# Optimization experiments

Measured on AMD Instinct MI355X. Metric: run time of the kernel, lower is better.

## Reference

```python
import math
import jax, jax.numpy as jnp
import numpy as np

G, NP, L = 256, 24, 3            # graphs, atoms per graph, GPS layers
C, TDIM, NFREQ, NT = 256, 256, 10, 100
EDIM = NFREQ * 2 * 3 + 9         # SinusoidsEmbedding.dim + lattice_input_dim = 69
N = G * NP                       # 6144 nodes
H = 4                            # attention heads


def _silu(x):
    return x * jax.nn.sigmoid(x)


def _bn(x, g, b):
    # BatchNorm1d, training-mode batch statistics (biased var), eps=1e-5
    m = x.mean(0)
    v = ((x - m) ** 2).mean(0)
    return (x - m) * jax.lax.rsqrt(v + 1e-5) * g + b


def _forward(t, frac_coords, lattice, type_emb, node_align_W, node_align_b,
             gine_edge_W, gine_edge_b, gine_W1, gine_b1, gine_W2, gine_b2,
             attn_in_W, attn_in_b, attn_out_W, attn_out_b,
             mlp_W1, mlp_b1, mlp_W2, mlp_b2,
             bn1_g, bn1_b, bn2_g, bn2_b, bn3_g, bn3_b, ln_g, ln_b,
             tro_W1, tro_b1, tro_W2, tro_b2,
             lat_W1, lat_b1, lat_W2, lat_b2, lat_W3,
             fc_W1, fc_b1, fc_W2, fc_b2, fc_W3,
             atom_types, node2graph, edge_src, edge_dst):
    # sinusoidal time embedding [G, TDIM], repeated per node
    half = TDIM // 2
    tf = jnp.exp(jnp.arange(half, dtype=jnp.float32) * (-math.log(10000.0) / (half - 1)))
    te = t[:, None] * tf[None, :]
    te = jnp.concatenate([jnp.sin(te), jnp.cos(te)], -1)
    time_emb = jnp.repeat(te, NP, axis=0)                      # [N, TDIM]
    x = jnp.concatenate([type_emb[atom_types], time_emb], 1) @ node_align_W + node_align_b

    # edge features: sinusoids of periodic frac diff + per-graph lattice
    fd = (frac_coords[edge_dst] - frac_coords[edge_src]) % 1.0  # [E,3]
    sf = 2.0 * math.pi * jnp.arange(NFREQ, dtype=jnp.float32)
    emb = (fd[..., None] * sf).reshape(-1, 3 * NFREQ)
    eattr = jnp.concatenate([jnp.sin(emb), jnp.cos(emb), lattice[node2graph[edge_src]]], 1)

    scale = 1.0 / math.sqrt(C // H)
    for l in range(L):
        # --- GINEConv: gather -> relu(x_j + edge_emb) -> scatter-add -> MLP ---
        eemb = eattr @ gine_edge_W[l] + gine_edge_b[l]          # [E, C]
        msg = jax.nn.relu(x[edge_src] + eemb)
        aggr = jax.ops.segment_sum(msg, edge_dst, num_segments=N)
        z = x + aggr                                            # (1+eps)*x, eps=0
        z = _silu(z @ gine_W1[l] + gine_b1[l]) @ gine_W2[l] + gine_b2[l]
        h1 = _bn(z + x, bn1_g[l], bn1_b[l])
        # --- dense-batched multihead self-attention (all graphs have NP nodes) ---
        xd = x.reshape(G, NP, C)
        qkv = xd @ attn_in_W[l] + attn_in_b[l]
        q, k, v = jnp.split(qkv, 3, axis=-1)
        q = q.reshape(G, NP, H, C // H).transpose(0, 2, 1, 3)
        k = k.reshape(G, NP, H, C // H).transpose(0, 2, 1, 3)
        v = v.reshape(G, NP, H, C // H).transpose(0, 2, 1, 3)
        a = jax.nn.softmax(jnp.einsum('ghqd,ghkd->ghqk', q, k) * scale, axis=-1)
        o = jnp.einsum('ghqk,ghkd->ghqd', a, v).transpose(0, 2, 1, 3).reshape(G, NP, C)
        o = (o @ attn_out_W[l] + attn_out_b[l]).reshape(N, C)
        h2 = _bn(o + x, bn2_g[l], bn2_b[l])
        # --- combine + MLP (GPSConv default: ReLU, dropout=0) ---
        out = h1 + h2
        out = out + jax.nn.relu(out @ mlp_W1[l] + mlp_b1[l]) @ mlp_W2[l] + mlp_b2[l]
        x = _bn(out, bn3_g[l], bn3_b[l])

    # final LayerNorm over feature dim
    m = x.mean(-1, keepdims=True)
    v = ((x - m) ** 2).mean(-1, keepdims=True)
    hn = (x - m) * jax.lax.rsqrt(v + 1e-5) * ln_g + ln_b

    # scatter-mean graph pooling
    cnt = jax.ops.segment_sum(jnp.ones((N, 1), hn.dtype), node2graph, num_segments=G)
    gf = jax.ops.segment_sum(hn, node2graph, num_segments=G) / cnt

    types_pred = _silu(hn @ tro_W1 + tro_b1) @ tro_W2 + tro_b2
    lattice_pred = _silu(_silu(gf @ lat_W1 + lat_b1) @ lat_W2 + lat_b2) @ lat_W3
    frac_pred = _silu(_silu(hn @ fc_W1 + fc_b1) @ fc_W2 + fc_b2) @ fc_W3
    return types_pred, lattice_pred, frac_pred


def setup_inputs() -> dict:
    key = jax.random.key(0)
    ki = iter(jax.random.split(key, 40))

    def nrm(shape, s=0.02):
        return jax.random.normal(next(ki), shape, jnp.float32) * s

    # block-diagonal fully-connected edges, dense_to_sparse row-major order
    g = np.repeat(np.arange(G), NP * NP)
    i = np.tile(np.repeat(np.arange(NP), NP), G)
    j = np.tile(np.tile(np.arange(NP), NP), G)
    inp = {
        "t": jax.random.uniform(next(ki), (G,), jnp.float32),
        "frac_coords": jax.random.uniform(next(ki), (N, 3), jnp.float32),
        "lattice": nrm((G, 9), 1.0),
        "type_emb": nrm((NT, C)),
        "node_align_W": nrm((C + TDIM, C)), "node_align_b": jnp.zeros((C,), jnp.float32),
        "gine_edge_W": nrm((L, EDIM, C)), "gine_edge_b": jnp.zeros((L, C), jnp.float32),
        "gine_W1": nrm((L, C, C)), "gine_b1": jnp.zeros((L, C), jnp.float32),
        "gine_W2": nrm((L, C, C)), "gine_b2": jnp.zeros((L, C), jnp.float32),
        "attn_in_W": nrm((L, C, 3 * C)), "attn_in_b": jnp.zeros((L, 3 * C), jnp.float32),
        "attn_out_W": nrm((L, C, C)), "attn_out_b": jnp.zeros((L, C), jnp.float32),
        "mlp_W1": nrm((L, C, 2 * C)), "mlp_b1": jnp.zeros((L, 2 * C), jnp.float32),
        "mlp_W2": nrm((L, 2 * C, C)), "mlp_b2": jnp.zeros((L, C), jnp.float32),
        "bn1_g": jnp.ones((L, C), jnp.float32), "bn1_b": jnp.zeros((L, C), jnp.float32),
        "bn2_g": jnp.ones((L, C), jnp.float32), "bn2_b": jnp.zeros((L, C), jnp.float32),
        "bn3_g": jnp.ones((L, C), jnp.float32), "bn3_b": jnp.zeros((L, C), jnp.float32),
        "ln_g": jnp.ones((C,), jnp.float32), "ln_b": jnp.zeros((C,), jnp.float32),
        "tro_W1": nrm((C, C // 2)), "tro_b1": jnp.zeros((C // 2,), jnp.float32),
        "tro_W2": nrm((C // 2, NT)), "tro_b2": jnp.zeros((NT,), jnp.float32),
        "lat_W1": nrm((C, C // 2)), "lat_b1": jnp.zeros((C // 2,), jnp.float32),
        "lat_W2": nrm((C // 2, C // 4)), "lat_b2": jnp.zeros((C // 4,), jnp.float32),
        "lat_W3": nrm((C // 4, 9)),
        "fc_W1": nrm((C, C // 2)), "fc_b1": jnp.zeros((C // 2,), jnp.float32),
        "fc_W2": nrm((C // 2, C // 4)), "fc_b2": jnp.zeros((C // 4,), jnp.float32),
        "fc_W3": nrm((C // 4, 3)),
        "atom_types": jax.random.randint(next(ki), (N,), 0, NT, jnp.int32),
        "node2graph": jnp.asarray(np.repeat(np.arange(G), NP), jnp.int32),
        "edge_src": jnp.asarray(g * NP + i, jnp.int32),
        "edge_dst": jnp.asarray(g * NP + j, jnp.int32),
    }
    return inp


def reference(t, frac_coords, lattice, type_emb, node_align_W, node_align_b,
              gine_edge_W, gine_edge_b, gine_W1, gine_b1, gine_W2, gine_b2,
              attn_in_W, attn_in_b, attn_out_W, attn_out_b,
              mlp_W1, mlp_b1, mlp_W2, mlp_b2,
              bn1_g, bn1_b, bn2_g, bn2_b, bn3_g, bn3_b, ln_g, ln_b,
              tro_W1, tro_b1, tro_W2, tro_b2,
              lat_W1, lat_b1, lat_W2, lat_b2, lat_W3,
              fc_W1, fc_b1, fc_W2, fc_b2, fc_W3,
              atom_types, node2graph, edge_src, edge_dst):
    return _forward(t, frac_coords, lattice, type_emb, node_align_W, node_align_b,
                    gine_edge_W, gine_edge_b, gine_W1, gine_b1, gine_W2, gine_b2,
                    attn_in_W, attn_in_b, attn_out_W, attn_out_b,
                    mlp_W1, mlp_b1, mlp_W2, mlp_b2,
                    bn1_g, bn1_b, bn2_g, bn2_b, bn3_g, bn3_b, ln_g, ln_b,
                    tro_W1, tro_b1, tro_W2, tro_b2,
                    lat_W1, lat_b1, lat_W2, lat_b2, lat_W3,
                    fc_W1, fc_b1, fc_W2, fc_b2, fc_W3,
                    atom_types, node2graph, edge_src, edge_dst)
```

## Files before the change

### kernel.cpp

```cpp
#include <hip/hip_runtime.h>
#include <hip/hip_bf16.h>
#include <math.h>

#define GG 256
#define NP 24
#define LL 3
#define CC 256
#define NN (GG*NP)
#define HH 4
#define DH 64

typedef __hip_bfloat16 bf;
typedef __attribute__((ext_vector_type(8))) short bfrag;
typedef __attribute__((ext_vector_type(4))) float ffrag;

__device__ __forceinline__ short pk(float x) {
    union { bf h; short s; } u; u.h = __float2bfloat16(x); return u.s;
}
__device__ __forceinline__ float b2f_s(short x) {
    union { short s; bf h; } u; u.s = x; return __bfloat162float(u.h);
}

typedef __attribute__((address_space(1))) const void gv_t;
typedef __attribute__((address_space(3))) void lv_t;

__global__ void signal_k(float* out, int n, float val) {
    int i = blockIdx.x * 256 + threadIdx.x;
    if (i < n) out[i] = val;
}

#define ETAB_ELEMS (GG * 24 * 24 * 64)
#define GEWTAB_BLKS (192 + (ETAB_ELEMS + 255) / 256)
#define BUILDA_BLKS ((NN * 512 + 255) / 256)

struct TArgs {
    const float* src[9];
    long dstOff[9];
    int K[9], N[9], L[9];
    int blk0[10];
};

__global__ void prep_all(TArgs a, bf* __restrict__ wt,
                         const float* __restrict__ geW, short* __restrict__ wh,
                         short* __restrict__ wl, const float* __restrict__ frac,
                         short* __restrict__ eh, short* __restrict__ el,
                         const float* __restrict__ t,
                         const float* __restrict__ type_emb,
                         const unsigned int* __restrict__ atoms,
                         float* __restrict__ A) {
    __shared__ int ok;
    int bid = blockIdx.x;
    int nT = a.blk0[9];
    if (bid < nT) {
        int s = 0;
        while (s < 8 && bid >= a.blk0[s + 1]) ++s;
        long idx = (long)(bid - a.blk0[s]) * 256 + threadIdx.x;
        int KN = a.K[s] * a.N[s];
        long sz = (long)KN * a.L[s];
        if (idx >= sz) return;
        int l = (int)(idx / KN);
        int rem = (int)(idx % KN);
        int k = rem / a.N[s], n = rem % a.N[s];
        wt[a.dstOff[s] + (long)l * KN + (long)n * a.K[s] + k] =
            __float2bfloat16(a.src[s][idx]);
    } else if (bid < nT + GEWTAB_BLKS) {
        int b2 = bid - nT;
        if (b2 < 192) {
            int idx = b2 * 256 + threadIdx.x;
            if (idx >= 49152) return;
            int k = idx & 63;
            int n = (idx >> 6) & 127;
            int half = (idx >> 13) & 1;
            int l = idx >> 14;
            float v = (k < 60) ? geW[(long)l * 69 * 256 + (long)k * 256 + half * 128 + n] : 0.f;
            short hi = pk(v);
            short lo = pk(v - b2f_s(hi));
            wh[idx] = hi;
            wl[idx] = lo;
        } else {
            int idx = (b2 - 192) * 256 + threadIdx.x;
            if (idx >= ETAB_ELEMS) return;
            int k = idx & 63;
            int rem = idx >> 6;
            int i = rem % 24;
            int rem2 = rem / 24;
            int j = rem2 % 24;
            int g = rem2 / 24;
            float val = 0.f;
            if (k < 60) {
                int r = (k < 30) ? k : k - 30;
                int d = r / 10, f = r % 10;
                float fd = frac[g * 72 + j * 3 + d] - frac[g * 72 + i * 3 + d];
                fd -= floorf(fd);
                float ang = 6.283185307179586f * (float)f * fd;
                val = (k < 30) ? sinf(ang) : cosf(ang);
            }
            short hi = pk(val);
            eh[idx] = hi;
            el[idx] = pk(val - b2f_s(hi));
        }
    } else {
        int b3 = bid - nT - GEWTAB_BLKS;
        if (threadIdx.x == 0) ok = 1;
        __syncthreads();
        if (atoms[2 * threadIdx.x + 1] != 0u) ok = 0;
        __syncthreads();
        int i64 = ok;
        int idx = b3 * 256 + threadIdx.x;
        if (idx >= NN * 512) return;
        int n = idx >> 9;
        int k = idx & 511;
        if (k < 256) {
            int aidx = i64 ? (int)atoms[2 * n] : (int)atoms[n];
            A[idx] = type_emb[(long)aidx * CC + k];
        } else {
            int d = k - 256;
            int g = n / NP;
            float tv = t[g];
            int dd = (d < 128) ? d : d - 128;
            float tf = expf(dd * (-9.210340371976184f / 127.0f));
            float ang = tv * tf;
            A[idx] = (d < 128) ? sinf(ang) : cosf(ang);
        }
    }
}

__global__ __launch_bounds__(256) void gemm_mfma(
        const float* __restrict__ A, const bf* __restrict__ Wt,
        const float* __restrict__ bias, const float* __restrict__ bias2,
        const float* __restrict__ res,
        float* __restrict__ C, int M, int K, int N, int act) {
    __shared__ __align__(16) short As[2][32 * 72];
    __shared__ __align__(16) short Bs[2][2][64 * 32];
    int tid = threadIdx.x;
    int lane = tid & 63, w = tid >> 6;
    int wm = w & 1, wn = w >> 1;
    int m0 = blockIdx.x * 32, n0 = blockIdx.y * 64;
    ffrag acc[2] = {};
    int sa_m = tid >> 3, sa_k = (tid & 7) << 3;
    int fr_row = lane & 15, quad = lane >> 4, fr_k = quad << 3;
    int brow = w * 16 + (lane >> 2);
    int bko = (lane & 3) << 3;
    const short* wsrc = (const short*)Wt + (long)(n0 + brow) * K + bko;

    {
        const float* Ap = A + (long)(m0 + sa_m) * K + sa_k;
        float4 a1 = *(const float4*)Ap;
        float4 a2 = *(const float4*)(Ap + 4);
        __builtin_amdgcn_global_load_lds((gv_t*)(wsrc), (lv_t*)(&Bs[0][0][w * 512]), 16, 0, 0);
        __builtin_amdgcn_global_load_lds((gv_t*)(wsrc + 32), (lv_t*)(&Bs[0][1][w * 512]), 16, 0, 0);
        short* ap = &As[0][sa_m * 72 + sa_k];
        ap[0] = pk(a1.x); ap[1] = pk(a1.y); ap[2] = pk(a1.z); ap[3] = pk(a1.w);
        ap[4] = pk(a2.x); ap[5] = pk(a2.y); ap[6] = pk(a2.z); ap[7] = pk(a2.w);
    }
    __syncthreads();

    int nk = K >> 6;
    int cur = 0;
    for (int i = 0; i < nk; ++i) {
        float4 a1n, a2n;
        bool more = (i + 1) < nk;
        if (more) {
            int kn = (i + 1) << 6;
            __builtin_amdgcn_global_load_lds((gv_t*)(wsrc + kn),
                (lv_t*)(&Bs[cur ^ 1][0][w * 512]), 16, 0, 0);
            __builtin_amdgcn_global_load_lds((gv_t*)(wsrc + kn + 32),
                (lv_t*)(&Bs[cur ^ 1][1][w * 512]), 16, 0, 0);
            const float* Ap = A + (long)(m0 + sa_m) * K + kn + sa_k;
            a1n = *(const float4*)Ap;
            a2n = *(const float4*)(Ap + 4);
        }
        bfrag af0  = *(const bfrag*)(&As[cur][(wm * 16 + fr_row) * 72 + fr_k]);
        bfrag af1  = *(const bfrag*)(&As[cur][(wm * 16 + fr_row) * 72 + 32 + fr_k]);
        bfrag bg00 = *(const bfrag*)(&Bs[cur][0][(wn * 32 + fr_row) * 32 + fr_k]);
        bfrag bg01 = *(const bfrag*)(&Bs[cur][0][(wn * 32 + 16 + fr_row) * 32 + fr_k]);
        bfrag bg10 = *(const bfrag*)(&Bs[cur][1][(wn * 32 + fr_row) * 32 + fr_k]);
        bfrag bg11 = *(const bfrag*)(&Bs[cur][1][(wn * 32 + 16 + fr_row) * 32 + fr_k]);
        acc[0] = __builtin_amdgcn_mfma_f32_16x16x32_bf16(af0, bg00, acc[0], 0, 0, 0);
        acc[1] = __builtin_amdgcn_mfma_f32_16x16x32_bf16(af0, bg01, acc[1], 0, 0, 0);
        acc[0] = __builtin_amdgcn_mfma_f32_16x16x32_bf16(af1, bg10, acc[0], 0, 0, 0);
        acc[1] = __builtin_amdgcn_mfma_f32_16x16x32_bf16(af1, bg11, acc[1], 0, 0, 0);
        if (more) {
            short* ap = &As[cur ^ 1][sa_m * 72 + sa_k];
            ap[0] = pk(a1n.x); ap[1] = pk(a1n.y); ap[2] = pk(a1n.z); ap[3] = pk(a1n.w);
            ap[4] = pk(a2n.x); ap[5] = pk(a2n.y); ap[6] = pk(a2n.z); ap[7] = pk(a2n.w);
        }
        __syncthreads();
        cur ^= 1;
    }

    int mbase = (lane >> 4) << 2;
#pragma unroll
    for (int nt = 0; nt < 2; ++nt) {
        int n = n0 + wn * 32 + nt * 16 + (lane & 15);
        float bv = bias ? ((bias2 && n >= 128) ? bias2[n - 128] : bias[n]) : 0.f;
#pragma unroll
        for (int r = 0; r < 4; ++r) {
            int m = m0 + wm * 16 + mbase + r;
            float v = acc[nt][r] + bv;
            if (act == 1) v = fmaxf(v, 0.f);
            else if (act == 2) v = v / (1.f + expf(-v));
            if (res) v += res[(long)m * N + n];
            C[(long)m * N + n] = v;
        }
    }
}

__device__ __forceinline__ void gemm_k_body(
        const float* __restrict__ A, int lda, int mA0,
        const float* __restrict__ W, const float* __restrict__ bias,
        float* __restrict__ Cf, int ldc, int mOut0,
        int n0, int K, int Nc, int act,
        float (*Asf)[64], float (*Bsf)[64], int tid) {
    int tx = tid & 15, ty = tid >> 4;
    float acc[4][4] = {{0.f}};
    int am = tid >> 2;
    int ak = (tid & 3) << 3;
    int bk = tid >> 4;
    int bn = (tid & 15) << 2;

    for (int k0 = 0; k0 < K; k0 += 32) {
        const float* Ap = A + (long)(mA0 + am) * lda + k0 + ak;
        float4 a1 = *(const float4*)Ap;
        float4 a2 = *(const float4*)(Ap + 4);
        float w1[4], w2[4];
#pragma unroll
        for (int u = 0; u < 4; ++u) {
            int n = n0 + bn + u;
            w1[u] = (n < Nc) ? W[(long)(k0 + bk) * Nc + n] : 0.f;
            w2[u] = (n < Nc) ? W[(long)(k0 + bk + 16) * Nc + n] : 0.f;
        }
        __syncthreads();
        Asf[ak + 0][am] = a1.x; Asf[ak + 1][am] = a1.y;
        Asf[ak + 2][am] = a1.z; Asf[ak + 3][am] = a1.w;
        Asf[ak + 4][am] = a2.x; Asf[ak + 5][am] = a2.y;
        Asf[ak + 6][am] = a2.z; Asf[ak + 7][am] = a2.w;
#pragma unroll
        for (int u = 0; u < 4; ++u) {
            Bsf[bk][bn + u] = w1[u];
            Bsf[bk + 16][bn + u] = w2[u];
        }
        __syncthreads();
#pragma unroll
        for (int k = 0; k < 32; ++k) {
            float4 a = *(const float4*)(&Asf[k][ty << 2]);
            float4 b = *(const float4*)(&Bsf[k][tx << 2]);
            acc[0][0] += a.x * b.x; acc[0][1] += a.x * b.y; acc[0][2] += a.x * b.z; acc[0][3] += a.x * b.w;
            acc[1][0] += a.y * b.x; acc[1][1] += a.y * b.y; acc[1][2] += a.y * b.z; acc[1][3] += a.y * b.w;
            acc[2][0] += a.z * b.x; acc[2][1] += a.z * b.y; acc[2][2] += a.z * b.z; acc[2][3] += a.z * b.w;
            acc[3][0] += a.w * b.x; acc[3][1] += a.w * b.y; acc[3][2] += a.w * b.z; acc[3][3] += a.w * b.w;
        }
    }
#pragma unroll
    for (int i = 0; i < 4; ++i) {
        int m = mOut0 + (ty << 2) + i;
#pragma unroll
        for (int j = 0; j < 4; ++j) {
            int n = n0 + (tx << 2) + j;
            if (n >= Nc) continue;
            float v = acc[i][j];
            if (bias) v += bias[n];
            if (act == 1) v = fmaxf(v, 0.f);
            else if (act == 2) v = v / (1.f + expf(-v));
            Cf[(long)m * ldc + n] = v;
        }
    }
}

__global__ __launch_bounds__(256) void tail_k(
        const float* __restrict__ s2, const float* __restrict__ s1,
        const float* __restrict__ W30, const float* __restrict__ b31,
        const float* __restrict__ W39, const float* __restrict__ b40,
        const float* __restrict__ W41,
        const float* __restrict__ lw1, const float* __restrict__ lb1,
        const float* __restrict__ lw2, const float* __restrict__ lb2,
        const float* __restrict__ lw3,
        float* __restrict__ out_types, float* __restrict__ out_lat,
        float* __restrict__ out_frac) {
    __shared__ __align__(16) float Asf[32][64];
    __shared__ __align__(16) float Bsf[32][64];
    __shared__ __align__(16) float Imm[64][64];
    __shared__ float gfl[256];
    __shared__ float h1s[128];
    __shared__ float h2s[64];
    int tid = threadIdx.x;
    int b = blockIdx.x;
    if (b < 192) {
        int bx = b >> 1, by = b & 1;
        gemm_k_body(s2, 256, bx * 64, W30, b31, out_types, 100, bx * 64,
                    by * 64, 128, 100, 0, Asf, Bsf, tid);
    } else if (b < 288) {
        int m0 = (b - 192) * 64;
        gemm_k_body(s2 + 128, 256, m0, W39, b40, &Imm[0][0], 64, 0,
                    0, 128, 64, 2, Asf, Bsf, tid);
        __syncthreads();
        gemm_k_body(&Imm[0][0], 64, 0, W41, nullptr, out_frac, 3, m0,
                    0, 64, 3, 0, Asf, Bsf, tid);
    } else {
        int g = b - 288, t = tid;
        {
            float s = 0.f;
            for (int j = 0; j < NP; ++j) s += s1[(long)(g * NP + j) * CC + t];
            gfl[t] = s * (1.f / 24.f);
        }
        __syncthreads();
        if (t < 128) {
            float acc = 0.f;
            for (int k = 0; k < 256; ++k) acc += gfl[k] * lw1[k * 128 + t];
            float v = acc;
            v += lb1[t];
            v = v / (1.f + expf(-v));
            h1s[t] = v;
        }
        __syncthreads();
        if (t < 64) {
            float acc = 0.f;
            for (int k = 0; k < 128; ++k) acc += h1s[k] * lw2[k * 64 + t];
            float v = acc;
            v += lb2[t];
            v = v / (1.f + expf(-v));
            h2s[t] = v;
        }
        __syncthreads();
        if (t < 9) {
            float acc = 0.f;
            for (int k = 0; k < 64; ++k) acc += h2s[k] * lw3[k * 9 + t];
            out_lat[(long)g * 9 + t] = acc;
        }
    }
}

#define MF(a, b, c) c = __builtin_amdgcn_mfma_f32_16x16x32_bf16(a, b, c, 0, 0, 0)

__device__ __forceinline__ void stage_etile(const short* __restrict__ ej_h,
                                            const short* __restrict__ ej_l,
                                            short* lds_base, int w, int lane) {
    {
        int c = w;
        const short* src = (c < 3) ? (ej_h + c * 512) : (ej_l + (c - 3) * 512);
        int doff = (c < 3) ? c * 512 : 2048 + (c - 3) * 512;
        __builtin_amdgcn_global_load_lds((gv_t*)(src + lane * 8),
                                         (lv_t*)(lds_base + doff), 16, 0, 0);
    }
    if (w < 2) {
        int c = w + 4;
        const short* src = ej_l + (c - 3) * 512;
        int doff = 2048 + (c - 3) * 512;
        __builtin_amdgcn_global_load_lds((gv_t*)(src + lane * 8),
                                         (lv_t*)(lds_base + doff), 16, 0, 0);
    }
}

__global__ __launch_bounds__(256, 4) void gine4(
        const float* __restrict__ x,
        const float* __restrict__ lattice, const float* __restrict__ geW,
        const float* __restrict__ geb, const short* __restrict__ gewt_h,
        const short* __restrict__ gewt_l, const short* __restrict__ et_h,
        const short* __restrict__ et_l, float* __restrict__ z, int l) {
    __shared__ __align__(16) float xls[24 * 132];
    __shared__ float basel[128];
    __shared__ __align__(16) short ebuf[8192];

    int tid = threadIdx.x;
    int lane = tid & 63, w = tid >> 6, quad = lane >> 4, l16 = lane & 15;
    int g = blockIdx.x >> 2;
    int half = (blockIdx.x >> 1) & 1;
    int jh = blockIdx.x & 1;

    {
        const float4* xg = (const float4*)x;
        for (int idx = tid; idx < 768; idx += 256) {
            int i = idx >> 5, c4 = idx & 31;
            ((float4*)(xls + i * 132))[c4] =
                xg[((long)(g * NP + i) * CC + half * 128) / 4 + c4];
        }
    }
    if (tid < 128) {
        int cg = half * 128 + tid;
        float bv = geb[(long)l * CC + cg];
#pragma unroll
        for (int q = 0; q < 9; ++q)
            bv += lattice[(long)g * 9 + q] * geW[(long)l * 69 * 256 + (long)(60 + q) * 256 + cg];
        basel[tid] = bv;
    }

    bfrag bh00, bh01, bh10, bh11, bl00, bl01, bl10, bl11;
    {
        long base = (long)(l * 2 + half) * 8192;
        int nrow0 = w * 32 + l16;
        int nrow1 = w * 32 + 16 + l16;
        const short* p0h = gewt_h + base + nrow0 * 64 + quad * 8;
        const short* p1h = gewt_h + base + nrow1 * 64 + quad * 8;
        const short* p0l = gewt_l + base + nrow0 * 64 + quad * 8;
        const short* p1l = gewt_l + base + nrow1 * 64 + quad * 8;
        bh00 = *(const bfrag*)(p0h);      bh01 = *(const bfrag*)(p0h + 32);
        bh10 = *(const bfrag*)(p1h);      bh11 = *(const bfrag*)(p1h + 32);
        bl00 = *(const bfrag*)(p0l);      bl01 = *(const bfrag*)(p0l + 32);
        bl10 = *(const bfrag*)(p1l);      bl11 = *(const bfrag*)(p1l + 32);
    }

    const short* ehg = et_h + (long)g * (24 * 24 * 64);
    const short* elg = et_l + (long)g * (24 * 24 * 64);
    int j0 = jh * 12;

    stage_etile(ehg + (long)j0 * 1536, elg + (long)j0 * 1536, ebuf, w, lane);
    __syncthreads();

    float bse0 = basel[w * 32 + l16];
    float bse1 = basel[w * 32 + 16 + l16];

    int cur = 0;
    for (int jc = 0; jc < 12; ++jc) {
        int j = j0 + jc;
        if (jc < 11) {
            stage_etile(ehg + (long)(j + 1) * 1536, elg + (long)(j + 1) * 1536,
                        ebuf + (cur ^ 1) * 4096, w, lane);
        }

        const short* eb = ebuf + cur * 4096;
        int r0 = l16 * 64 + quad * 8;
        int r1 = (16 + l16) * 64 + quad * 8;
        bfrag ah00 = *(const bfrag*)(eb + r0);
        bfrag ah01 = *(const bfrag*)(eb + r0 + 32);
        bfrag ah10 = *(const bfrag*)(eb + r1);
        bfrag ah11 = *(const bfrag*)(eb + r1 + 32);
        bfrag al00 = *(const bfrag*)(eb + 2048 + r0);
        bfrag al01 = *(const bfrag*)(eb + 2048 + r0 + 32);
        bfrag al10 = *(const bfrag*)(eb + 2048 + r1);
        bfrag al11 = *(const bfrag*)(eb + 2048 + r1 + 32);

        ffrag a00 = {}, a01 = {}, a10 = {}, a11 = {};
        MF(ah00, bh00, a00); MF(ah00, bl00, a00); MF(al00, bh00, a00);
        MF(ah00, bh10, a01); MF(ah00, bl10, a01); MF(al00, bh10, a01);
        MF(ah01, bh01, a00); MF(ah01, bl01, a00); MF(al01, bh01, a00);
        MF(ah01, bh11, a01); MF(ah01, bl11, a01); MF(al01, bh11, a01);
        MF(ah10, bh00, a10); MF(ah10, bl00, a10); MF(al10, bh00, a10);
        MF(ah10, bh10, a11); MF(ah10, bl10, a11); MF(al10, bh10, a11);
        MF(ah11, bh01, a10); MF(ah11, bl01, a10); MF(al11, bh01, a10);
        MF(ah11, bh11, a11); MF(ah11, bl11, a11); MF(al11, bh11, a11);

#pragma unroll
        for (int nt = 0; nt < 2; ++nt) {
            int cl = w * 32 + nt * 16 + l16;
            float bse = nt ? bse1 : bse0;
            ffrag am0 = nt ? a01 : a00;
            ffrag am1 = nt ? a11 : a10;
            float part = 0.f;
            {
                int ibase = quad * 4;
#pragma unroll
                for (int r = 0; r < 4; ++r) {
                    float xv = xls[(ibase + r) * 132 + cl];
                    part += fmaxf(xv + bse + am0[r], 0.f);
                }
            }
            if (quad < 2) {
                int ibase = 16 + quad * 4;
#pragma unroll
                for (int r = 0; r < 4; ++r) {
                    float xv = xls[(ibase + r) * 132 + cl];
                    part += fmaxf(xv + bse + am1[r], 0.f);
                }
            }
            part += __shfl_xor(part, 16);
            part += __shfl_xor(part, 32);
            if (lane < 16)
                z[(long)(g * NP + j) * CC + half * 128 + cl] = xls[j * 132 + cl] + part;
        }
        __syncthreads();
        cur ^= 1;
    }
}

__global__ void bn_stats1(const float* __restrict__ in, float* __restrict__ part) {
    int c = threadIdx.x, b = blockIdx.x;
    float s = 0.f, q = 0.f;
    for (int r = 0; r < 64; ++r) {
        float v = in[(long)(b * 64 + r) * CC + c];
        s += v; q += v * v;
    }
    part[b * 512 + c] = s;
    part[b * 512 + 256 + c] = q;
}
__global__ __launch_bounds__(256) void bn_apply2(
        const float* __restrict__ in, const float* __restrict__ part,
        const float* __restrict__ gma, const float* __restrict__ bta,
        const float* __restrict__ add, float* __restrict__ out) {
    int c = threadIdx.x;
    float s = 0.f, q = 0.f;
    for (int b = 0; b < 96; ++b) { s += part[b * 512 + c]; q += part[b * 512 + 256 + c]; }
    float m = s / (float)NN;
    float var = q / (float)NN - m * m;
    float stats_c = m;
    float stats_rs = rsqrtf(var + 1e-5f);
    float gc = gma[c], bc = bta[c];
    for (int r = blockIdx.x; r < NN; r += 768) {
        long idx = (long)r * CC + c;
        float v = (in[idx] - stats_c) * stats_rs * gc + bc;
        if (add) v += add[idx];
        out[idx] = v;
    }
}

__global__ __launch_bounds__(256, 2) void attn2(const float* __restrict__ qkv,
                                                float* __restrict__ o) {
    __shared__ __align__(16) float Kl[24 * 4 * 68];
    __shared__ __align__(16) float Vl[24 * 4 * 68];
    __shared__ float S[4 * 24 * 25];
    int tid = threadIdx.x, g = blockIdx.x;

    const float4* qkv4 = (const float4*)(qkv + (long)g * NP * 768);
    for (int idx = tid; idx < 24 * 128; idx += 256) {
        int row = idx >> 7;
        int c4 = idx & 127;
        int isV = c4 >> 6;
        int cc = c4 & 63;
        int h = cc >> 4, d4 = cc & 15;
        float4 val = qkv4[row * 192 + 64 + c4];
        float* dst = (isV ? Vl : Kl) + (row * 4 + h) * 68 + d4 * 4;
        *(float4*)dst = val;
    }
    __syncthreads();

    if (tid < 96) {
        int h = tid & 3, i = tid >> 2;
        const float4* qp = (const float4*)(qkv + ((long)(g * NP + i)) * 768 + h * 64);
        float4 q[16];
#pragma unroll
        for (int k = 0; k < 16; ++k) q[k] = qp[k];
        float sc[24];
        float mx = -1e30f;
        for (int j = 0; j < 24; ++j) {
            const float4* kp = (const float4*)(Kl + (j * 4 + h) * 68);
            float da = 0.f, db = 0.f;
#pragma unroll
            for (int k = 0; k < 16; k += 2) {
                float4 kv = kp[k];
                da += q[k].x * kv.x; da += q[k].y * kv.y;
                da += q[k].z * kv.z; da += q[k].w * kv.w;
                float4 kv2 = kp[k + 1];
                db += q[k + 1].x * kv2.x; db += q[k + 1].y * kv2.y;
                db += q[k + 1].z * kv2.z; db += q[k + 1].w * kv2.w;
            }
            float s = (da + db) * 0.125f;
            sc[j] = s;
            mx = fmaxf(mx, s);
        }
        float sum = 0.f;
#pragma unroll
        for (int j = 0; j < 24; ++j) { float p = expf(sc[j] - mx); sc[j] = p; sum += p; }
        float inv = 1.f / sum;
#pragma unroll
        for (int j = 0; j < 24; ++j) S[(h * 24 + i) * 25 + j] = sc[j] * inv;
    }
    __syncthreads();

    int h = tid >> 6, d = tid & 63;
    for (int i = 0; i < 24; ++i) {
        const float* Sp = S + (h * 24 + i) * 25;
        float a0 = 0.f, a1 = 0.f;
#pragma unroll
        for (int j = 0; j < 24; j += 2) {
            a0 += Sp[j] * Vl[(j * 4 + h) * 68 + d];
            a1 += Sp[j + 1] * Vl[((j + 1) * 4 + h) * 68 + d];
        }
        o[(long)(g * NP + i) * CC + h * 64 + d] = a0 + a1;
    }
}

__global__ __launch_bounds__(256) void ln_kernel(const float* __restrict__ x,
        const float* __restrict__ gma, const float* __restrict__ bta,
        float* __restrict__ out) {
    __shared__ float red[256];
    int n = blockIdx.x, c = threadIdx.x;
    float v = x[(long)n * CC + c];
    red[c] = v;
    __syncthreads();
    for (int s = 128; s > 0; s >>= 1) { if (c < s) red[c] += red[c + s]; __syncthreads(); }
    float m = red[0] * (1.f / 256.f);
    __syncthreads();
    float dv = v - m;
    red[c] = dv * dv;
    __syncthreads();
    for (int s = 128; s > 0; s >>= 1) { if (c < s) red[c] += red[c + s]; __syncthreads(); }
    float var = red[0] * (1.f / 256.f);
    out[(long)n * CC + c] = dv * rsqrtf(var + 1e-5f) * gma[c] + bta[c];
}

static void gemmM(hipStream_t st, const float* A, const bf* Wt, const float* bias,
                  const float* bias2, const float* res, float* Cf,
                  int M, int K, int N, int act) {
    dim3 grid(M / 32, N / 64);
    gemm_mfma<<<grid, 256, 0, st>>>(A, Wt, bias, bias2, res, Cf, M, K, N, act);
}

static void run_bn(hipStream_t st, const float* in, float* part,
                   const float* g_, const float* b_, const float* add, float* out) {
    bn_stats1<<<96, 256, 0, st>>>(in, part);
    bn_apply2<<<768, 256, 0, st>>>(in, part, g_, b_, add, out);
}

extern "C" void kernel_launch(void* const* d_in, const int* in_sizes, int n_in,
                              void* d_out, int out_size, void* d_ws, size_t ws_size,
                              hipStream_t stream) {
    float* out = (float*)d_out;
    int sigN = out_size < 256 ? out_size : 256;

    static const int EXP_SIZES[46] = {
        256, 18432, 2304, 25600, 131072, 256, 52992, 768, 196608, 768,
        196608, 768, 589824, 2304, 196608, 768, 393216, 1536, 393216, 768,
        768, 768, 768, 768, 768, 768, 256, 256, 32768, 128,
        12800, 100, 32768, 128, 8192, 64, 576, 32768, 128, 8192,
        64, 192, 6144, 6144, 147456, 147456 };
    if (n_in != 46) { signal_k<<<1, 256, 0, stream>>>(out, sigN, 3000.f + 8.f * n_in); return; }
    for (int i = 0; i < 46; ++i)
        if (in_sizes[i] != EXP_SIZES[i]) { signal_k<<<1, 256, 0, stream>>>(out, sigN, 512.f + 8.f * i); return; }
    if (out_size != NN * 100 + GG * 9 + NN * 3) { signal_k<<<1, 256, 0, stream>>>(out, sigN, 7777.f); return; }

    char* base = (char*)d_ws;
    float* f32a = (float*)(base + 256);
    float* x  = f32a;
    float* s1 = x  + (size_t)NN * 256;
    float* s2 = s1 + (size_t)NN * 256;
    float* big = s2 + (size_t)NN * 256;
    float* s3 = big + (size_t)NN * 512;
    float* part = big + (size_t)NN * 768;
    float* stats = part + 96 * 512;
    float* gf  = stats + 512;
    float* l1b = gf + GG * 256;
    float* l2b = l1b + GG * 128;
    bf* wt = (bf*)(l2b + GG * 64);
    const long O_NA = 0, O_G1 = 131072, O_G2 = 327680, O_AI = 524288,
               O_AO = 1114112, O_M1 = 1310720, O_M2 = 1703936,
               O_TRO = 2097152, O_FC = 2129920, WT_TOT = 2162688;
    short* gewt_h = (short*)(wt + WT_TOT);
    short* gewt_l = gewt_h + 49152;
    short* et_h = gewt_l + 49152;
    short* et_l = et_h + (ETAB_ELEMS + 1024);
    size_t REQ = 256 + ((size_t)NN * 1536 + 96 * 512 + 512 + GG * 448) * 4
               + WT_TOT * 2 + 49152 * 2 * 2
               + ((size_t)ETAB_ELEMS + 1024) * 2 * 2;
    if (ws_size < REQ) { signal_k<<<1, 256, 0, stream>>>(out, sigN, 9999.f); return; }

    const float* t       = (const float*)d_in[0];
    const float* frac    = (const float*)d_in[1];
    const float* lattice = (const float*)d_in[2];
    const float* type_emb = (const float*)d_in[3];

    int nTblk;
    {
        TArgs ta;
        const int srcIdx[9] = {4, 8, 10, 12, 14, 16, 18, 28, 37};
        const long dof[9]  = {O_NA, O_G1, O_G2, O_AI, O_AO, O_M1, O_M2, O_TRO, O_FC};
        const int Ks[9] = {512, 256, 256, 256, 256, 256, 512, 256, 256};
        const int Ns[9] = {256, 256, 256, 768, 256, 512, 256, 128, 128};
        const int Ls[9] = {1, 3, 3, 3, 3, 3, 3, 1, 1};
        int blk = 0;
        for (int s = 0; s < 9; ++s) {
            ta.src[s] = (const float*)d_in[srcIdx[s]];
            ta.dstOff[s] = dof[s];
            ta.K[s] = Ks[s]; ta.N[s] = Ns[s]; ta.L[s] = Ls[s];
            ta.blk0[s] = blk;
            blk += (Ks[s] * Ns[s] * Ls[s] + 255) / 256;
        }
        ta.blk0[9] = blk;
        nTblk = blk;
        prep_all<<<nTblk + GEWTAB_BLKS + BUILDA_BLKS, 256, 0, stream>>>(
            ta, wt, (const float*)d_in[6], gewt_h, gewt_l, frac, et_h, et_l,
            t, type_emb, (const unsigned int*)d_in[42], big);
    }

    gemmM(stream, big, wt + O_NA, (const float*)d_in[5], nullptr, nullptr, x, NN, 512, 256, 0);

    for (int l = 0; l < LL; ++l) {
        gine4<<<GG * 4, 256, 0, stream>>>(x, lattice,
            (const float*)d_in[6], (const float*)d_in[7], gewt_h, gewt_l,
            et_h, et_l, s1, l);
        gemmM(stream, s1, wt + O_G1 + (long)l * 65536, (const float*)d_in[9]  + l * 256, nullptr, nullptr, s2, NN, 256, 256, 2);
        gemmM(stream, s2, wt + O_G2 + (long)l * 65536, (const float*)d_in[11] + l * 256, nullptr, x, s3, NN, 256, 256, 0);
        run_bn(stream, s3, part, (const float*)d_in[20] + l * 256, (const float*)d_in[21] + l * 256, nullptr, s2);
        gemmM(stream, x, wt + O_AI + (long)l * 196608, (const float*)d_in[13] + l * 768, nullptr, nullptr, big, NN, 256, 768, 0);
        attn2<<<GG, 256, 0, stream>>>(big, s1);
        gemmM(stream, s1, wt + O_AO + (long)l * 65536, (const float*)d_in[15] + l * 256, nullptr, x, s3, NN, 256, 256, 0);
        run_bn(stream, s3, part, (const float*)d_in[22] + l * 256, (const float*)d_in[23] + l * 256, s2, s1);
        gemmM(stream, s1, wt + O_M1 + (long)l * 131072, (const float*)d_in[17] + l * 512, nullptr, nullptr, big, NN, 256, 512, 1);
        gemmM(stream, big, wt + O_M2 + (long)l * 131072, (const float*)d_in[19] + l * 256, nullptr, s1, s3, NN, 512, 256, 0);
        run_bn(stream, s3, part, (const float*)d_in[24] + l * 256, (const float*)d_in[25] + l * 256, nullptr, x);
    }

    ln_kernel<<<NN, 256, 0, stream>>>(x, (const float*)d_in[26], (const float*)d_in[27], s1);

    gemmM(stream, s1, wt + O_TRO, (const float*)d_in[29], (const float*)d_in[38],
          nullptr, s2, NN, 256, 256, 2);
    tail_k<<<544, 256, 0, stream>>>(s2, s1,
        (const float*)d_in[30], (const float*)d_in[31],
        (const float*)d_in[39], (const float*)d_in[40], (const float*)d_in[41],
        (const float*)d_in[32], (const float*)d_in[33],
        (const float*)d_in[34], (const float*)d_in[35], (const float*)d_in[36],
        out, out + (size_t)NN * 100, out + (size_t)NN * 100 + GG * 9);
}
```

Baseline: 676.2 us.

## Merge BN1 apply with attention in-projection GEMM into one launch

Runs the attention in-projection GEMM on x and the BatchNorm apply pass of the GINE branch as separate block ranges of a single kernel, since the two are independent. This removes one launch and lets the elementwise BN work overlap with GEMM blocks, with each BN block recomputing the per-channel statistics from the partial sums. It also skips the sin/cos evaluation for zero-frequency edge table entries, and it compacts the workspace layout by dropping unused buffers.

```diff
diff --git a/kernel.cpp b/kernel.cpp
--- a/kernel.cpp
+++ b/kernel.cpp
@@ -90,10 +90,14 @@
             if (k < 60) {
                 int r = (k < 30) ? k : k - 30;
                 int d = r / 10, f = r % 10;
-                float fd = frac[g * 72 + j * 3 + d] - frac[g * 72 + i * 3 + d];
-                fd -= floorf(fd);
-                float ang = 6.283185307179586f * (float)f * fd;
-                val = (k < 30) ? sinf(ang) : cosf(ang);
+                if (f == 0) {
+                    val = (k < 30) ? 0.f : 1.f;
+                } else {
+                    float fd = frac[g * 72 + j * 3 + d] - frac[g * 72 + i * 3 + d];
+                    fd -= floorf(fd);
+                    float ang = 6.283185307179586f * (float)f * fd;
+                    val = (k < 30) ? sinf(ang) : cosf(ang);
+                }
             }
             short hi = pk(val);
             eh[idx] = hi;
@@ -125,17 +129,14 @@
     }
 }
 
-__global__ __launch_bounds__(256) void gemm_mfma(
+__device__ __forceinline__ void gemm_mfma_body(
         const float* __restrict__ A, const bf* __restrict__ Wt,
         const float* __restrict__ bias, const float* __restrict__ bias2,
-        const float* __restrict__ res,
-        float* __restrict__ C, int M, int K, int N, int act) {
-    __shared__ __align__(16) short As[2][32 * 72];
-    __shared__ __align__(16) short Bs[2][2][64 * 32];
-    int tid = threadIdx.x;
+        const float* __restrict__ res, float* __restrict__ C,
+        int K, int N, int act, int m0, int n0,
+        short (*As)[32 * 72], short (*Bs)[2][64 * 32], int tid) {
     int lane = tid & 63, w = tid >> 6;
     int wm = w & 1, wn = w >> 1;
-    int m0 = blockIdx.x * 32, n0 = blockIdx.y * 64;
     ffrag acc[2] = {};
     int sa_m = tid >> 3, sa_k = (tid & 7) << 3;
     int fr_row = lane & 15, quad = lane >> 4, fr_k = quad << 3;
@@ -202,6 +203,50 @@
             else if (act == 2) v = v / (1.f + expf(-v));
             if (res) v += res[(long)m * N + n];
             C[(long)m * N + n] = v;
+        }
+    }
+}
+
+__global__ __launch_bounds__(256) void gemm_mfma(
+        const float* __restrict__ A, const bf* __restrict__ Wt,
+        const float* __restrict__ bias, const float* __restrict__ bias2,
+        const float* __restrict__ res,
+        float* __restrict__ C, int M, int K, int N, int act) {
+    __shared__ __align__(16) short As[2][32 * 72];
+    __shared__ __align__(16) short Bs[2][2][64 * 32];
+    gemm_mfma_body(A, Wt, bias, bias2, res, C, K, N, act,
+                   blockIdx.x * 32, blockIdx.y * 64, As, Bs, threadIdx.x);
+}
+
+__global__ __launch_bounds__(256) void apply_ai(
+        const float* __restrict__ Ag, const bf* __restrict__ Wt,
+        const float* __restrict__ bias, float* __restrict__ C, int K, int N,
+        const float* __restrict__ in, const float* __restrict__ part,
+        const float* __restrict__ gma, const float* __restrict__ bta,
+        const float* __restrict__ add, float* __restrict__ out) {
+    __shared__ __align__(16) short As[2][32 * 72];
+    __shared__ __align__(16) short Bs[2][2][64 * 32];
+    int b = blockIdx.x;
+    int nb = N / 64;
+    int ng = (NN / 32) * nb;
+    if (b < ng) {
+        gemm_mfma_body(Ag, Wt, bias, nullptr, nullptr, C, K, N, 0,
+                       (b / nb) * 32, (b % nb) * 64, As, Bs, threadIdx.x);
+    } else {
+        int bb = b - ng;
+        int c = threadIdx.x;
+        float s = 0.f, q = 0.f;
+        for (int b2 = 0; b2 < 96; ++b2) { s += part[b2 * 512 + c]; q += part[b2 * 512 + 256 + c]; }
+        float m = s / (float)NN;
+        float var = q / (float)NN - m * m;
+        float stats_c = m;
+        float stats_rs = rsqrtf(var + 1e-5f);
+        float gc = gma[c], bc = bta[c];
+        for (int r = bb; r < NN; r += 768) {
+            long idx = (long)r * CC + c;
+            float v = (in[idx] - stats_c) * stats_rs * gc + bc;
+            if (add) v += add[idx];
+            out[idx] = v;
         }
     }
 }
@@ -623,13 +668,9 @@
     float* s1 = x  + (size_t)NN * 256;
     float* s2 = s1 + (size_t)NN * 256;
     float* big = s2 + (size_t)NN * 256;
-    float* s3 = big + (size_t)NN * 512;
-    float* part = big + (size_t)NN * 768;
-    float* stats = part + 96 * 512;
-    float* gf  = stats + 512;
-    float* l1b = gf + GG * 256;
-    float* l2b = l1b + GG * 128;
-    bf* wt = (bf*)(l2b + GG * 64);
+    float* s3 = big + (size_t)NN * 768;
+    float* part = s3 + (size_t)NN * 256;
+    bf* wt = (bf*)(part + 96 * 512);
     const long O_NA = 0, O_G1 = 131072, O_G2 = 327680, O_AI = 524288,
                O_AO = 1114112, O_M1 = 1310720, O_M2 = 1703936,
                O_TRO = 2097152, O_FC = 2129920, WT_TOT = 2162688;
@@ -637,7 +678,7 @@
     short* gewt_l = gewt_h + 49152;
     short* et_h = gewt_l + 49152;
     short* et_l = et_h + (ETAB_ELEMS + 1024);
-    size_t REQ = 256 + ((size_t)NN * 1536 + 96 * 512 + 512 + GG * 448) * 4
+    size_t REQ = 256 + ((size_t)NN * 1792 + 96 * 512) * 4
                + WT_TOT * 2 + 49152 * 2 * 2
                + ((size_t)ETAB_ELEMS + 1024) * 2 * 2;
     if (ws_size < REQ) { signal_k<<<1, 256, 0, stream>>>(out, sigN, 9999.f); return; }
@@ -678,8 +719,11 @@
             et_h, et_l, s1, l);
         gemmM(stream, s1, wt + O_G1 + (long)l * 65536, (const float*)d_in[9]  + l * 256, nullptr, nullptr, s2, NN, 256, 256, 2);
         gemmM(stream, s2, wt + O_G2 + (long)l * 65536, (const float*)d_in[11] + l * 256, nullptr, x, s3, NN, 256, 256, 0);
-        run_bn(stream, s3, part, (const float*)d_in[20] + l * 256, (const float*)d_in[21] + l * 256, nullptr, s2);
-        gemmM(stream, x, wt + O_AI + (long)l * 196608, (const float*)d_in[13] + l * 768, nullptr, nullptr, big, NN, 256, 768, 0);
+        bn_stats1<<<96, 256, 0, stream>>>(s3, part);
+        apply_ai<<<(NN / 32) * 12 + 768, 256, 0, stream>>>(
+            x, wt + O_AI + (long)l * 196608, (const float*)d_in[13] + l * 768, big, 256, 768,
+            s3, part, (const float*)d_in[20] + l * 256, (const float*)d_in[21] + l * 256,
+            nullptr, s2);
         attn2<<<GG, 256, 0, stream>>>(big, s1);
         gemmM(stream, s1, wt + O_AO + (long)l * 65536, (const float*)d_in[15] + l * 256, nullptr, x, s3, NN, 256, 256, 0);
         run_bn(stream, s3, part, (const float*)d_in[22] + l * 256, (const float*)d_in[23] + l * 256, s2, s1);
```

After: 654.0 us, median of 2. 3.3% less time.
